# Kernel tuning notes

Hardware: AMD Instinct MI355X
Metric: run time of the kernel (lower is better)

## Reference

```python
import jax, jax.numpy as jnp
import numpy as np

C_CURV = 1.0
EPS = 1e-5            # bound_eps from source
MAX_NORM = (1.0 - 1e-5) / (C_CURV ** 0.5)  # Poincare ball projection radius


def _conv3x3(x, w, b):
    # x: (N,Cin,H,W), w: (Cout,Cin,3,3), padding=1 -> SAME
    y = jax.lax.conv_general_dilated(
        x, w, window_strides=(1, 1), padding=((1, 1), (1, 1)),
        dimension_numbers=('NCHW', 'OIHW', 'NCHW'))
    return y + b[None, :, None, None]


def _maxpool2(x):
    return jax.lax.reduce_window(x, -jnp.inf, jax.lax.max,
                                 (1, 1, 2, 2), (1, 1, 2, 2), 'VALID')


def _hyp_mlr(x, w, b):
    # x: (N,D), w: hyperplane_normals (K,D), b: hyperplane_offsets (K,D)
    c = C_CURV
    sqrt_c = c ** 0.5
    x2 = jnp.sum(x * x, axis=-1, keepdims=True)          # (N,1)
    b2 = jnp.sum(b * b, axis=-1)                          # (K,)
    w_norm = jnp.linalg.norm(w, axis=-1)                  # (K,)
    inner_x_b = x @ (-b.T)                                # (N,K)
    a_num = 1.0 + 2.0 * c * inner_x_b + c * x2            # (N,K)
    b_num = 1.0 - c * b2                                  # (K,)
    denom = 1.0 + 2.0 * c * inner_x_b + (c * c) * (x2 * b2[None, :])
    alpha = a_num / jnp.maximum(denom, EPS)
    beta = b_num[None, :] / denom                         # raw denom, as in source
    mob2 = alpha ** 2 * b2[None, :] + 2.0 * alpha * beta * inner_x_b + beta ** 2 * x2
    sq = jnp.sqrt(mob2)
    normalizer = jnp.where(sq > MAX_NORM, MAX_NORM / jnp.maximum(sq, EPS),
                           jnp.ones_like(mob2))
    mob2 = jnp.where(sq < MAX_NORM, mob2, jnp.full_like(mob2, MAX_NORM ** 2))
    wn = w / jnp.maximum(jnp.linalg.norm(w, axis=-1, keepdims=True), 1e-12)
    hyperplane = alpha * jnp.sum(wn * (-b), axis=-1)[None, :] + beta * (x @ wn.T)
    hyperplane = hyperplane * normalizer
    asinh_in = 2.0 * sqrt_c * hyperplane / jnp.maximum(1.0 - c * mob2, EPS)
    scaler = 2.0 / jnp.maximum(1.0 - c * b2, EPS)         # (K,)
    return (1.0 / sqrt_c) * (scaler * w_norm)[None, :] * jnp.arcsinh(asinh_in)


def setup_inputs() -> dict:
    key = jax.random.key(0)
    ks = jax.random.split(key, 8)
    N, D, K = 4096, 32, 10
    x = jax.random.normal(ks[0], (N, 1, 28, 28), dtype=jnp.float32)
    conv1_w = jax.random.normal(ks[1], (32, 1, 3, 3), dtype=jnp.float32) * 0.1
    conv1_b = jnp.zeros((32,), dtype=jnp.float32)
    conv2_w = jax.random.normal(ks[2], (64, 32, 3, 3), dtype=jnp.float32) * 0.05
    conv2_b = jnp.zeros((64,), dtype=jnp.float32)
    fc_w = jax.random.normal(ks[3], (D, 7 * 7 * 64), dtype=jnp.float32) * 0.02
    fc_b = jnp.zeros((D,), dtype=jnp.float32)
    hyp_w = jax.random.normal(ks[4], (K, D), dtype=jnp.float32) * 0.05
    hyp_b = jnp.zeros((K, D), dtype=jnp.float32)
    return dict(x=x, conv1_w=conv1_w, conv1_b=conv1_b, conv2_w=conv2_w,
                conv2_b=conv2_b, fc_w=fc_w, fc_b=fc_b, hyp_w=hyp_w, hyp_b=hyp_b)


def reference(x, conv1_w, conv1_b, conv2_w, conv2_b, fc_w, fc_b, hyp_w, hyp_b):
    h = _maxpool2(jax.nn.relu(_conv3x3(x, conv1_w, conv1_b)))   # (N,32,14,14)
    h = _maxpool2(jax.nn.relu(_conv3x3(h, conv2_w, conv2_b)))   # (N,64,7,7)
    h = h.reshape(h.shape[0], -1)                                # (N,3136)
    h = h @ fc_w.T + fc_b                                        # (N,32)
    return _hyp_mlr(h, hyp_w, hyp_b)                             # (N,10)
```

## Files before the change

kernel.cpp:

```cpp
#include <hip/hip_runtime.h>
#include <math.h>

#define EPSV 1e-5f

typedef _Float16 f16x8 __attribute__((ext_vector_type(8)));
typedef _Float16 f16x4 __attribute__((ext_vector_type(4)));
typedef float f32x4 __attribute__((ext_vector_type(4)));

__global__ __launch_bounds__(256) void prep_weights(
    const float* __restrict__ w1, const float* __restrict__ b1,
    const float* __restrict__ w2, const float* __restrict__ fw,
    _Float16* __restrict__ w2t_hi, _Float16* __restrict__ w2t_lo,
    _Float16* __restrict__ fw_hi,  _Float16* __restrict__ fw_lo,
    _Float16* __restrict__ w1p_hi, _Float16* __restrict__ w1p_lo)
{
    int idx = blockIdx.x * 256 + threadIdx.x;
    if (idx < 18432) {
        int off = idx >> 11;
        int rem = idx & 2047;
        int oc = rem >> 5, ic = rem & 31;
        float v = w2[(oc * 32 + ic) * 9 + off];
        _Float16 hx = (_Float16)v;
        w2t_hi[idx] = hx;
        w2t_lo[idx] = (_Float16)(v - (float)hx);
    } else if (idx < 18432 + 100352) {
        int j = idx - 18432;
        float v = fw[j];
        _Float16 hx = (_Float16)v;
        fw_hi[j] = hx;
        fw_lo[j] = (_Float16)(v - (float)hx);
    } else if (idx < 18432 + 100352 + 1024) {
        int j = idx - (18432 + 100352);
        int oc = j >> 5, k = j & 31;
        float v = (k < 9) ? w1[oc * 9 + k] : ((k == 9) ? b1[oc] : 0.f);
        _Float16 hx = (_Float16)v;
        w1p_hi[j] = hx;
        w1p_lo[j] = (_Float16)(v - (float)hx);
    }
}

template<int ROW0, int NROWS, int P2OFF>
__device__ __forceinline__ void conv2_half(
    const _Float16* __restrict__ w2t_hi, const _Float16* __restrict__ w2t_lo,
    const _Float16* Bbuf_hi, const _Float16* Bbuf_lo,
    _Float16* Fhi, _Float16* Flo,
    int ocb, int cl, int kg, const float* bias, bool wlane, int px2)
{
    f32x4 acc[NROWS];
    #pragma unroll
    for (int r = 0; r < NROWS; ++r) acc[r] = (f32x4){0.f, 0.f, 0.f, 0.f};

    #pragma unroll 1
    for (int off = 0; off < 9; ++off) {
        int ky = off / 3, kx = off - ky * 3;
        f16x8 a_hi = *(const f16x8*)(w2t_hi + ((size_t)off * 64 + ocb + cl) * 32 + kg * 8);
        f16x8 a_lo = *(const f16x8*)(w2t_lo + ((size_t)off * 64 + ocb + cl) * 32 + kg * 8);
        const int base = (kg * 256 + (ROW0 + ky) * 16 + (cl + kx)) * 8;
        #pragma unroll
        for (int py = 0; py < NROWS; ++py) {
            f16x8 b_hi = *(const f16x8*)(Bbuf_hi + base + py * 128);
            f16x8 b_lo = *(const f16x8*)(Bbuf_lo + base + py * 128);
            acc[py] = __builtin_amdgcn_mfma_f32_16x16x32_f16(a_hi, b_hi, acc[py], 0, 0, 0);
            acc[py] = __builtin_amdgcn_mfma_f32_16x16x32_f16(a_lo, b_hi, acc[py], 0, 0, 0);
            acc[py] = __builtin_amdgcn_mfma_f32_16x16x32_f16(a_hi, b_lo, acc[py], 0, 0, 0);
        }
    }
    #pragma unroll
    for (int p = 0; p < NROWS / 2; ++p) {
        f32x4 r0 = acc[2 * p], r1 = acc[2 * p + 1];
        #pragma unroll
        for (int r = 0; r < 4; ++r) {
            float v0 = fmaxf(r0[r], __shfl_xor(r0[r], 1));
            float v1 = fmaxf(r1[r], __shfl_xor(r1[r], 1));
            float m = fmaxf(fmaxf(v0, v1) + bias[r], 0.f);
            _Float16 mh = (_Float16)m;
            _Float16 ml = (_Float16)(m - (float)mh);
            if (wlane) {
                int o = (ocb + kg * 4 + r) * 49 + (P2OFF + p) * 7 + px2;
                Fhi[o] = mh; Flo[o] = ml;
            }
        }
    }
}

__global__ __launch_bounds__(256, 3) void conv_fused(
    const float* __restrict__ x,
    const _Float16* __restrict__ w1p_hi,
    const _Float16* __restrict__ w1p_lo,
    const _Float16* __restrict__ w2t_hi,
    const _Float16* __restrict__ w2t_lo,
    const float* __restrict__ b2,
    _Float16* __restrict__ feat_hi,
    _Float16* __restrict__ feat_lo)
{
    __shared__ float4 smem4[3060];
    unsigned* in_pad  = (unsigned*)smem4;
    _Float16* Bbuf_hi = (_Float16*)((char*)smem4 + 3600);
    _Float16* Bbuf_lo = (_Float16*)((char*)smem4 + 19984);
    _Float16* Fhi     = (_Float16*)((char*)smem4 + 36416);
    _Float16* Flo     = (_Float16*)((char*)smem4 + 42688);

    const int tid  = threadIdx.x;
    const int lane = tid & 63;
    const int wave = tid >> 6;
    const int kg   = lane >> 4;
    const int cl   = lane & 15;
    const int n    = blockIdx.x;

    for (int i = tid; i < 116; i += 256) {
        int yy, xx;
        if (i < 30)       { yy = 0;          xx = i; }
        else if (i < 60)  { yy = 29;         xx = i - 30; }
        else if (i < 88)  { yy = i - 60 + 1; xx = 0; }
        else              { yy = i - 88 + 1; xx = 29; }
        in_pad[yy * 30 + xx] = 0u;
    }
    const float* xin = x + (size_t)n * 784;
    for (int i = tid; i < 784; i += 256) {
        int yy = i / 28, xx = i - yy * 28;
        float v = xin[i];
        _Float16 hx = (_Float16)v;
        _Float16 lx = (_Float16)(v - (float)hx);
        unsigned hb = *(const unsigned short*)&hx;
        unsigned lb = *(const unsigned short*)&lx;
        in_pad[(yy + 1) * 30 + (xx + 1)] = hb | (lb << 16);
    }
    {
        int* zp = (int*)Bbuf_hi;
        for (int i = tid; i < 8192; i += 256) zp[i] = 0;
    }
    __syncthreads();

    {
        f16x8 a1h[2], a1l[2];
        #pragma unroll
        for (int m = 0; m < 2; ++m) {
            a1h[m] = *(const f16x8*)(w1p_hi + (m * 16 + cl) * 32 + kg * 8);
            a1l[m] = *(const f16x8*)(w1p_lo + (m * 16 + cl) * 32 + kg * 8);
        }
        const int o0 = (kg == 0) ? 0  : ((kg == 1) ? 62 : 0);
        const int o1 = (kg == 0) ? 1  : 0;
        const int o2 = (kg == 0) ? 2  : 0;
        const int o3 = (kg == 0) ? 30 : 0;
        const int o4 = (kg == 0) ? 31 : 0;
        const int o5 = (kg == 0) ? 32 : 0;
        const int o6 = (kg == 0) ? 60 : 0;
        const int o7 = (kg == 0) ? 61 : 0;

        const bool wr = ((cl & 1) == 0) && (cl < 14);

        #pragma unroll 1
        for (int rp = wave; rp < 14; rp += 4) {
            #pragma unroll
            for (int hx = 0; hx < 2; ++hx) {
                const int xcol = hx * 14 + cl;
                f16x8 bh[2], bl[2];
                #pragma unroll
                for (int r2 = 0; r2 < 2; ++r2) {
                    const int base = (2 * rp + r2) * 30 + xcol;
                    unsigned v0 = in_pad[base + o0], v1 = in_pad[base + o1];
                    unsigned v2 = in_pad[base + o2], v3 = in_pad[base + o3];
                    unsigned v4 = in_pad[base + o4], v5 = in_pad[base + o5];
                    unsigned v6 = in_pad[base + o6], v7 = in_pad[base + o7];
                    unsigned h01 = (v0 & 0xFFFFu) | (v1 << 16);
                    unsigned h23 = (v2 & 0xFFFFu) | (v3 << 16);
                    unsigned h45 = (v4 & 0xFFFFu) | (v5 << 16);
                    unsigned h67 = (v6 & 0xFFFFu) | (v7 << 16);
                    unsigned l01 = (v0 >> 16) | (v1 & 0xFFFF0000u);
                    unsigned l23 = (v2 >> 16) | (v3 & 0xFFFF0000u);
                    unsigned l45 = (v4 >> 16) | (v5 & 0xFFFF0000u);
                    unsigned l67 = (v6 >> 16) | (v7 & 0xFFFF0000u);
                    if (kg == 1) {
                        h01 = (h01 & 0xFFFFu) | 0x3C000000u;
                        l01 = (l01 & 0xFFFFu);
                        h23 = h45 = h67 = 0u; l23 = l45 = l67 = 0u;
                    } else if (kg >= 2) {
                        h01 = h23 = h45 = h67 = 0u;
                        l01 = l23 = l45 = l67 = 0u;
                    }
                    union { unsigned u[4]; f16x8 v; } uh, ul;
                    uh.u[0] = h01; uh.u[1] = h23; uh.u[2] = h45; uh.u[3] = h67;
                    ul.u[0] = l01; ul.u[1] = l23; ul.u[2] = l45; ul.u[3] = l67;
                    bh[r2] = uh.v; bl[r2] = ul.v;
                }
                #pragma unroll
                for (int m = 0; m < 2; ++m) {
                    f32x4 a0 = (f32x4){0.f, 0.f, 0.f, 0.f};
                    f32x4 a1 = (f32x4){0.f, 0.f, 0.f, 0.f};
                    a0 = __builtin_amdgcn_mfma_f32_16x16x32_f16(a1h[m], bh[0], a0, 0, 0, 0);
                    a0 = __builtin_amdgcn_mfma_f32_16x16x32_f16(a1l[m], bh[0], a0, 0, 0, 0);
                    a0 = __builtin_amdgcn_mfma_f32_16x16x32_f16(a1h[m], bl[0], a0, 0, 0, 0);
                    a1 = __builtin_amdgcn_mfma_f32_16x16x32_f16(a1h[m], bh[1], a1, 0, 0, 0);
                    a1 = __builtin_amdgcn_mfma_f32_16x16x32_f16(a1l[m], bh[1], a1, 0, 0, 0);
                    a1 = __builtin_amdgcn_mfma_f32_16x16x32_f16(a1h[m], bl[1], a1, 0, 0, 0);
                    float pv[4];
                    #pragma unroll
                    for (int r = 0; r < 4; ++r) {
                        float vp = fmaxf(a0[r], a1[r]);
                        float hp = fmaxf(vp, __shfl_xor(vp, 1));
                        pv[r] = fmaxf(hp, 0.f);
                    }
                    union { unsigned short s[4]; f16x4 v; } ph, pl;
                    #pragma unroll
                    for (int r = 0; r < 4; ++r) {
                        _Float16 mh = (_Float16)pv[r];
                        _Float16 ml = (_Float16)(pv[r] - (float)mh);
                        ph.s[r] = *(const unsigned short*)&mh;
                        pl.s[r] = *(const unsigned short*)&ml;
                    }
                    if (wr) {
                        const int px2 = hx * 7 + (cl >> 1);
                        const int cell = ((m * 2 + (kg >> 1)) * 256 +
                                          (rp + 1) * 16 + (px2 + 1)) * 8 + (kg & 1) * 4;
                        *(f16x4*)(Bbuf_hi + cell) = ph.v;
                        *(f16x4*)(Bbuf_lo + cell) = pl.v;
                    }
                }
            }
        }
    }
    __syncthreads();

    const int ocb = wave * 16;
    float bias[4];
    #pragma unroll
    for (int r = 0; r < 4; ++r) bias[r] = b2[ocb + kg * 4 + r];
    const bool wlane = ((cl & 1) == 0) && (cl < 14);
    const int px2 = cl >> 1;

    conv2_half<0, 8, 0>(w2t_hi, w2t_lo, Bbuf_hi, Bbuf_lo, Fhi, Flo,
                        ocb, cl, kg, bias, wlane, px2);
    conv2_half<8, 6, 4>(w2t_hi, w2t_lo, Bbuf_hi, Bbuf_lo, Fhi, Flo,
                        ocb, cl, kg, bias, wlane, px2);
    __syncthreads();

    unsigned* gh = (unsigned*)(feat_hi + (size_t)n * 3136);
    unsigned* gl = (unsigned*)(feat_lo + (size_t)n * 3136);
    const unsigned* sh = (const unsigned*)Fhi;
    const unsigned* sl = (const unsigned*)Flo;
    for (int i = tid; i < 1568; i += 256) { gh[i] = sh[i]; gl[i] = sl[i]; }
}

__global__ __launch_bounds__(256) void fc_mlr(
    const _Float16* __restrict__ feat_hi, const _Float16* __restrict__ feat_lo,
    const _Float16* __restrict__ fw_hi,   const _Float16* __restrict__ fw_lo,
    const float* __restrict__ fb,
    const float* __restrict__ hw,
    const float* __restrict__ hb,
    float* __restrict__ out)
{
    __shared__ float part[4][64][9];
    __shared__ float Ht[16][33];

    const int tid  = threadIdx.x;
    const int lane = tid & 63;
    const int wave = tid >> 6;
    const int kg = lane >> 4, cl = lane & 15;
    const int m0 = blockIdx.x * 16;

    const int start = wave * 25 - (wave == 3 ? 1 : 0);
    const int nstep = (wave < 2) ? 25 : 24;
    const size_t koff = (size_t)start * 32 + kg * 8;

    const _Float16* ah  = feat_hi + (size_t)(m0 + cl) * 3136 + koff;
    const _Float16* al  = feat_lo + (size_t)(m0 + cl) * 3136 + koff;
    const _Float16* b0h = fw_hi + (size_t)cl * 3136 + koff;
    const _Float16* b0l = fw_lo + (size_t)cl * 3136 + koff;
    const _Float16* b1h = fw_hi + (size_t)(16 + cl) * 3136 + koff;
    const _Float16* b1l = fw_lo + (size_t)(16 + cl) * 3136 + koff;

    f32x4 acc0 = {0.f, 0.f, 0.f, 0.f}, acc1 = {0.f, 0.f, 0.f, 0.f};
    for (int s = 0; s < nstep; ++s) {
        int k0 = s * 32;
        f16x8 vah = *(const f16x8*)(ah + k0);
        f16x8 val_ = *(const f16x8*)(al + k0);
        f16x8 v0h = *(const f16x8*)(b0h + k0);
        f16x8 v0l = *(const f16x8*)(b0l + k0);
        f16x8 v1h = *(const f16x8*)(b1h + k0);
        f16x8 v1l = *(const f16x8*)(b1l + k0);
        acc0 = __builtin_amdgcn_mfma_f32_16x16x32_f16(vah, v0h, acc0, 0, 0, 0);
        acc0 = __builtin_amdgcn_mfma_f32_16x16x32_f16(val_, v0h, acc0, 0, 0, 0);
        acc0 = __builtin_amdgcn_mfma_f32_16x16x32_f16(vah, v0l, acc0, 0, 0, 0);
        acc1 = __builtin_amdgcn_mfma_f32_16x16x32_f16(vah, v1h, acc1, 0, 0, 0);
        acc1 = __builtin_amdgcn_mfma_f32_16x16x32_f16(val_, v1h, acc1, 0, 0, 0);
        acc1 = __builtin_amdgcn_mfma_f32_16x16x32_f16(vah, v1l, acc1, 0, 0, 0);
    }
    #pragma unroll
    for (int r = 0; r < 4; ++r) {
        part[wave][lane][r]     = acc0[r];
        part[wave][lane][4 + r] = acc1[r];
    }
    __syncthreads();

    #pragma unroll
    for (int jj = 0; jj < 2; ++jj) {
        int j = tid + jj * 256;
        int col = j & 31, row = j >> 5;
        int l  = ((row >> 2) << 4) + (col & 15);
        int rr = ((col >= 16) ? 4 : 0) + (row & 3);
        float s = part[0][l][rr] + part[1][l][rr] + part[2][l][rr] + part[3][l][rr];
        Ht[row][col] = s + fb[col];
    }
    __syncthreads();

    if (tid < 160) {
        int im = tid / 10, k = tid - im * 10;
        const float* xr = &Ht[im][0];
        const float* wr = hw + k * 32;
        const float* br = hb + k * 32;
        float x2 = 0.f, b2s = 0.f, ww = 0.f, xb = 0.f, xw = 0.f, wb = 0.f;
        #pragma unroll
        for (int i = 0; i < 32; ++i) {
            float xi = xr[i], wi = wr[i], bi = br[i];
            x2 += xi * xi;  b2s += bi * bi;  ww += wi * wi;
            xb += xi * bi;  xw += xi * wi;   wb += wi * bi;
        }
        float w_norm = sqrtf(ww);
        float wnc = fmaxf(w_norm, 1e-12f);
        float inner = -xb;
        float a_num = 1.f + 2.f * inner + x2;
        float b_num = 1.f - b2s;
        float den = 1.f + 2.f * inner + x2 * b2s;
        float alpha = a_num / fmaxf(den, EPSV);
        float beta = b_num / den;
        float mob2 = alpha * alpha * b2s + 2.f * alpha * beta * inner + beta * beta * x2;
        float sq = sqrtf(mob2);
        const float MAXN = (float)(1.0 - 1e-5);
        const float MAXN2 = (float)((1.0 - 1e-5) * (1.0 - 1e-5));
        float normalizer = (sq > MAXN) ? (MAXN / fmaxf(sq, EPSV)) : 1.f;
        float mob2c = (sq < MAXN) ? mob2 : MAXN2;
        float hyper = (alpha * (-wb) + beta * xw) / wnc;
        hyper *= normalizer;
        float asin_in = 2.f * hyper / fmaxf(1.f - mob2c, EPSV);
        float scaler = 2.f / fmaxf(1.f - b2s, EPSV);
        out[(size_t)m0 * 10 + tid] = scaler * w_norm * asinhf(asin_in);
    }
}

extern "C" void kernel_launch(void* const* d_in, const int* in_sizes, int n_in,
                              void* d_out, int out_size, void* d_ws, size_t ws_size,
                              hipStream_t stream) {
    const float* x   = (const float*)d_in[0];
    const float* w1  = (const float*)d_in[1];
    const float* b1  = (const float*)d_in[2];
    const float* w2  = (const float*)d_in[3];
    const float* b2  = (const float*)d_in[4];
    const float* fw  = (const float*)d_in[5];
    const float* fb  = (const float*)d_in[6];
    const float* hw  = (const float*)d_in[7];
    const float* hb  = (const float*)d_in[8];
    float* out = (float*)d_out;

    const int N = 4096;
    char* ws = (char*)d_ws;
    _Float16* feat_hi = (_Float16*)ws;
    _Float16* feat_lo = (_Float16*)(ws + 25690112);
    _Float16* w2t_hi  = (_Float16*)(ws + 51380224);
    _Float16* w2t_lo  = (_Float16*)(ws + 51417088);
    _Float16* fw_hi   = (_Float16*)(ws + 51453952);
    _Float16* fw_lo   = (_Float16*)(ws + 51654656);
    _Float16* w1p_hi  = (_Float16*)(ws + 51855360);
    _Float16* w1p_lo  = (_Float16*)(ws + 51857408);

    prep_weights<<<(18432 + 100352 + 1024 + 255) / 256, 256, 0, stream>>>(
        w1, b1, w2, fw, w2t_hi, w2t_lo, fw_hi, fw_lo, w1p_hi, w1p_lo);
    conv_fused<<<N, 256, 0, stream>>>(x, w1p_hi, w1p_lo, w2t_hi, w2t_lo, b2,
                                      feat_hi, feat_lo);
    fc_mlr<<<N / 16, 256, 0, stream>>>(feat_hi, feat_lo, fw_hi, fw_lo, fb, hw, hb, out);
}
```

Measured before the change: 156.2 us.

## Alias pooled-feature LDS onto dead input buffer, zero only halo, widen FC to 8 waves

```diff
diff --git a/kernel.cpp b/kernel.cpp
--- a/kernel.cpp
+++ b/kernel.cpp
@@ -39,12 +39,11 @@
     }
 }
 
-template<int ROW0, int NROWS, int P2OFF>
+template<int ROW0, int NROWS>
 __device__ __forceinline__ void conv2_half(
     const _Float16* __restrict__ w2t_hi, const _Float16* __restrict__ w2t_lo,
     const _Float16* Bbuf_hi, const _Float16* Bbuf_lo,
-    _Float16* Fhi, _Float16* Flo,
-    int ocb, int cl, int kg, const float* bias, bool wlane, int px2)
+    int ocb, int cl, int kg, const float* bias, float pool[][4])
 {
     f32x4 acc[NROWS];
     #pragma unroll
@@ -72,18 +71,12 @@
         for (int r = 0; r < 4; ++r) {
             float v0 = fmaxf(r0[r], __shfl_xor(r0[r], 1));
             float v1 = fmaxf(r1[r], __shfl_xor(r1[r], 1));
-            float m = fmaxf(fmaxf(v0, v1) + bias[r], 0.f);
-            _Float16 mh = (_Float16)m;
-            _Float16 ml = (_Float16)(m - (float)mh);
-            if (wlane) {
-                int o = (ocb + kg * 4 + r) * 49 + (P2OFF + p) * 7 + px2;
-                Fhi[o] = mh; Flo[o] = ml;
-            }
-        }
-    }
-}
-
-__global__ __launch_bounds__(256, 3) void conv_fused(
+            pool[p][r] = fmaxf(fmaxf(v0, v1) + bias[r], 0.f);
+        }
+    }
+}
+
+__global__ __launch_bounds__(256, 4) void conv_fused(
     const float* __restrict__ x,
     const _Float16* __restrict__ w1p_hi,
     const _Float16* __restrict__ w1p_lo,
@@ -93,12 +86,12 @@
     _Float16* __restrict__ feat_hi,
     _Float16* __restrict__ feat_lo)
 {
-    __shared__ float4 smem4[3060];
+    __shared__ float4 smem4[2276];
     unsigned* in_pad  = (unsigned*)smem4;
     _Float16* Bbuf_hi = (_Float16*)((char*)smem4 + 3600);
     _Float16* Bbuf_lo = (_Float16*)((char*)smem4 + 19984);
-    _Float16* Fhi     = (_Float16*)((char*)smem4 + 36416);
-    _Float16* Flo     = (_Float16*)((char*)smem4 + 42688);
+    _Float16* Fhi     = (_Float16*)smem4;
+    _Float16* Flo     = Fhi + 3136;
 
     const int tid  = threadIdx.x;
     const int lane = tid & 63;
@@ -125,9 +118,16 @@
         unsigned lb = *(const unsigned short*)&lx;
         in_pad[(yy + 1) * 30 + (xx + 1)] = hb | (lb << 16);
     }
-    {
-        int* zp = (int*)Bbuf_hi;
-        for (int i = tid; i < 8192; i += 256) zp[i] = 0;
+    if (tid < 240) {
+        int icg = tid / 60, j = tid - icg * 60;
+        int row, col;
+        if (j < 16)      { row = 0;      col = j; }
+        else if (j < 32) { row = 15;     col = j - 16; }
+        else if (j < 46) { row = j - 31; col = 0; }
+        else             { row = j - 45; col = 15; }
+        int c = (icg * 256 + row * 16 + col) * 8;
+        *(f32x4*)(Bbuf_hi + c) = (f32x4){0.f, 0.f, 0.f, 0.f};
+        *(f32x4*)(Bbuf_lo + c) = (f32x4){0.f, 0.f, 0.f, 0.f};
     }
     __syncthreads();
 
@@ -225,13 +225,27 @@
     float bias[4];
     #pragma unroll
     for (int r = 0; r < 4; ++r) bias[r] = b2[ocb + kg * 4 + r];
+
+    float pooled[7][4];
+    conv2_half<0, 8>(w2t_hi, w2t_lo, Bbuf_hi, Bbuf_lo, ocb, cl, kg, bias, &pooled[0]);
+    conv2_half<8, 6>(w2t_hi, w2t_lo, Bbuf_hi, Bbuf_lo, ocb, cl, kg, bias, &pooled[4]);
+    __syncthreads();
+
     const bool wlane = ((cl & 1) == 0) && (cl < 14);
     const int px2 = cl >> 1;
-
-    conv2_half<0, 8, 0>(w2t_hi, w2t_lo, Bbuf_hi, Bbuf_lo, Fhi, Flo,
-                        ocb, cl, kg, bias, wlane, px2);
-    conv2_half<8, 6, 4>(w2t_hi, w2t_lo, Bbuf_hi, Bbuf_lo, Fhi, Flo,
-                        ocb, cl, kg, bias, wlane, px2);
+    if (wlane) {
+        #pragma unroll
+        for (int p = 0; p < 7; ++p) {
+            #pragma unroll
+            for (int r = 0; r < 4; ++r) {
+                float m = pooled[p][r];
+                _Float16 mh = (_Float16)m;
+                _Float16 ml = (_Float16)(m - (float)mh);
+                int o = (ocb + kg * 4 + r) * 49 + p * 7 + px2;
+                Fhi[o] = mh; Flo[o] = ml;
+            }
+        }
+    }
     __syncthreads();
 
     unsigned* gh = (unsigned*)(feat_hi + (size_t)n * 3136);
@@ -241,7 +255,7 @@
     for (int i = tid; i < 1568; i += 256) { gh[i] = sh[i]; gl[i] = sl[i]; }
 }
 
-__global__ __launch_bounds__(256) void fc_mlr(
+__global__ __launch_bounds__(512) void fc_mlr(
     const _Float16* __restrict__ feat_hi, const _Float16* __restrict__ feat_lo,
     const _Float16* __restrict__ fw_hi,   const _Float16* __restrict__ fw_lo,
     const float* __restrict__ fb,
@@ -249,7 +263,7 @@
     const float* __restrict__ hb,
     float* __restrict__ out)
 {
-    __shared__ float part[4][64][9];
+    __shared__ float part[8][64][9];
     __shared__ float Ht[16][33];
 
     const int tid  = threadIdx.x;
@@ -258,8 +272,8 @@
     const int kg = lane >> 4, cl = lane & 15;
     const int m0 = blockIdx.x * 16;
 
-    const int start = wave * 25 - (wave == 3 ? 1 : 0);
-    const int nstep = (wave < 2) ? 25 : 24;
+    const int start = (wave < 2) ? wave * 13 : 26 + (wave - 2) * 12;
+    const int nstep = (wave < 2) ? 13 : 12;
     const size_t koff = (size_t)start * 32 + kg * 8;
 
     const _Float16* ah  = feat_hi + (size_t)(m0 + cl) * 3136 + koff;
@@ -292,13 +306,13 @@
     }
     __syncthreads();
 
-    #pragma unroll
-    for (int jj = 0; jj < 2; ++jj) {
-        int j = tid + jj * 256;
-        int col = j & 31, row = j >> 5;
+    {
+        int col = tid & 31, row = tid >> 5;
         int l  = ((row >> 2) << 4) + (col & 15);
         int rr = ((col >= 16) ? 4 : 0) + (row & 3);
-        float s = part[0][l][rr] + part[1][l][rr] + part[2][l][rr] + part[3][l][rr];
+        float s = 0.f;
+        #pragma unroll
+        for (int w = 0; w < 8; ++w) s += part[w][l][rr];
         Ht[row][col] = s + fb[col];
     }
     __syncthreads();
@@ -366,5 +380,5 @@
         w1, b1, w2, fw, w2t_hi, w2t_lo, fw_hi, fw_lo, w1p_hi, w1p_lo);
     conv_fused<<<N, 256, 0, stream>>>(x, w1p_hi, w1p_lo, w2t_hi, w2t_lo, b2,
                                       feat_hi, feat_lo);
-    fc_mlr<<<N / 16, 256, 0, stream>>>(feat_hi, feat_lo, fw_hi, fw_lo, fb, hw, hb, out);
-}
+    fc_mlr<<<N / 16, 512, 0, stream>>>(feat_hi, feat_lo, fw_hi, fw_lo, fb, hw, hb, out);
+}
```

Result: faster. 141.8 us (-9.3%).
